# Kernel optimization log

Hardware: AMD Instinct MI355X
Metric: run time of the kernel (lower is better)

Reference implementation:

```python
import jax, jax.numpy as jnp
import numpy as np

B, T, C = 4, 2048, 2048
H, G = 16, 4            # num_heads, gqa_factor
HKV = H // G            # kv heads = 4
D = C // H              # head_dim = 128
KV = HKV * D            # kv_embed_dim = 512


def setup_inputs() -> dict:
    key = jax.random.key(0)
    ks = jax.random.split(key, 6)
    w_scale = (2.0 / (C + C)) ** 0.5  # xavier-uniform-ish std
    return {
        "query": jax.random.normal(ks[0], (B, T, C), jnp.float32),
        "key": jax.random.normal(ks[1], (B, T, C), jnp.float32),
        "value": jax.random.normal(ks[2], (B, T, C), jnp.float32),
        "in_proj_weight": jax.random.normal(ks[3], (C + 2 * KV, C), jnp.float32) * w_scale,
        "in_proj_bias": jnp.zeros((C + 2 * KV,), jnp.float32),
        "out_proj_weight": jax.random.normal(ks[4], (C, C), jnp.float32) * w_scale,
        "out_proj_bias": jnp.zeros((C,), jnp.float32),
    }


def reference(query, key, value, in_proj_weight, in_proj_bias, out_proj_weight, out_proj_bias):
    # split fused QKV projection (rows: [C | KV | KV])
    qw, kw, vw = in_proj_weight[:C], in_proj_weight[C:C + KV], in_proj_weight[C + KV:]
    qb, kb, vb = in_proj_bias[:C], in_proj_bias[C:C + KV], in_proj_bias[C + KV:]

    xq = query @ qw.T + qb          # (B,T,C)
    xk = key @ kw.T + kb            # (B,T,KV)
    xv = value @ vw.T + vb          # (B,T,KV)

    # (B,T,G,Hkv,D) -> (B,G,Hkv,T,D)
    xq = xq.reshape(B, T, G, HKV, D).transpose(0, 2, 3, 1, 4)
    # (B,T,Hkv,D) -> (B,Hkv,T,D); broadcast over G in attention
    xk = xk.reshape(B, T, HKV, D).transpose(0, 2, 1, 3)
    xv = xv.reshape(B, T, HKV, D).transpose(0, 2, 1, 3)

    scale = 1.0 / jnp.sqrt(jnp.asarray(D, xq.dtype))
    scores = jnp.einsum("bghtd,bhsd->bghts", xq, xk) * scale  # (B,G,Hkv,T,T)
    causal = jnp.tril(jnp.ones((T, T), bool))
    scores = jnp.where(causal, scores, jnp.finfo(scores.dtype).min)
    attn = jax.nn.softmax(scores, axis=-1)

    xo = jnp.einsum("bghts,bhsd->bghtd", attn, xv)            # (B,G,Hkv,T,D)
    xo = xo.transpose(0, 3, 1, 2, 4).reshape(B, T, C)          # (B,T,C)
    return xo @ out_proj_weight.T + out_proj_bias
```

## Files before the change

### kernel.cpp

```cpp
#include <hip/hip_runtime.h>
#include <hip/hip_bf16.h>
#include <stdint.h>

#define B_ 4
#define T_ 2048
#define C_ 2048
#define H_ 16
#define HKV_ 4
#define D_ 128
#define KV_ 512

typedef __attribute__((ext_vector_type(8))) short bf16x8;
typedef __attribute__((ext_vector_type(4))) float f32x4;

__device__ __forceinline__ unsigned short f2bf(float f) {
    union { float f; unsigned int u; } c;
    c.f = f;
    unsigned int u = c.u;
    u += 0x7FFFu + ((u >> 16) & 1u);
    return (unsigned short)(u >> 16);
}

__global__ __launch_bounds__(256)
void f32_to_bf16(const float* __restrict__ src, unsigned short* __restrict__ dst, int n4)
{
    int i = blockIdx.x * 256 + threadIdx.x;
    if (i < n4) {
        float4 v = ((const float4*)src)[i];
        ushort4 o;
        o.x = f2bf(v.x); o.y = f2bf(v.y); o.z = f2bf(v.z); o.w = f2bf(v.w);
        ((ushort4*)dst)[i] = o;
    }
}

template <typename OutT, bool TRANS>
__global__ __launch_bounds__(256)
void gemm_bt_bias(const __hip_bfloat16* __restrict__ A,
                  const __hip_bfloat16* __restrict__ W,
                  const float* __restrict__ bias,
                  OutT* __restrict__ Cmat,
                  int M, int N, int K)
{
    __shared__ __align__(16) __hip_bfloat16 lA[128 * 32];
    __shared__ __align__(16) __hip_bfloat16 lB[128 * 32];

    const int tid  = threadIdx.x;
    const int wave = tid >> 6;
    const int lane = tid & 63;
    const int m0 = blockIdx.x * 128;
    const int n0 = blockIdx.y * 128;
    const int wm = (wave >> 1) * 64;
    const int wn = (wave & 1) * 64;
    const int srow = lane >> 2;
    const int scol = (lane & 3) * 8;
    const int quad = lane >> 4;
    const int r16  = lane & 15;

    f32x4 acc[4][4];
#pragma unroll
    for (int i = 0; i < 4; ++i)
#pragma unroll
        for (int j = 0; j < 4; ++j)
            acc[i][j] = (f32x4){0.f, 0.f, 0.f, 0.f};

    const __hip_bfloat16* gA = A + (size_t)(m0 + wave * 16 + srow) * K + scol;
    const __hip_bfloat16* gB = W + (size_t)(n0 + wave * 16 + srow) * K + scol;

    for (int k0 = 0; k0 < K; k0 += 32) {
        __builtin_amdgcn_global_load_lds(
            (const __attribute__((address_space(1))) void*)(gA + k0),
            (__attribute__((address_space(3))) void*)(lA + wave * 16 * 32), 16, 0, 0);
        __builtin_amdgcn_global_load_lds(
            (const __attribute__((address_space(1))) void*)(gA + (size_t)64 * K + k0),
            (__attribute__((address_space(3))) void*)(lA + (64 + wave * 16) * 32), 16, 0, 0);
        __builtin_amdgcn_global_load_lds(
            (const __attribute__((address_space(1))) void*)(gB + k0),
            (__attribute__((address_space(3))) void*)(lB + wave * 16 * 32), 16, 0, 0);
        __builtin_amdgcn_global_load_lds(
            (const __attribute__((address_space(1))) void*)(gB + (size_t)64 * K + k0),
            (__attribute__((address_space(3))) void*)(lB + (64 + wave * 16) * 32), 16, 0, 0);
        __syncthreads();

        bf16x8 af[4], bfr[4];
#pragma unroll
        for (int i = 0; i < 4; ++i)
            af[i] = *(const bf16x8*)(lA + (wm + i * 16 + r16) * 32 + quad * 8);
#pragma unroll
        for (int j = 0; j < 4; ++j)
            bfr[j] = *(const bf16x8*)(lB + (wn + j * 16 + r16) * 32 + quad * 8);
#pragma unroll
        for (int i = 0; i < 4; ++i)
#pragma unroll
            for (int j = 0; j < 4; ++j)
                acc[i][j] = __builtin_amdgcn_mfma_f32_16x16x32_bf16(
                    af[i], bfr[j], acc[i][j], 0, 0, 0);
        __syncthreads();
    }

#pragma unroll
    for (int i = 0; i < 4; ++i) {
        const int row = m0 + wm + i * 16 + quad * 4;
#pragma unroll
        for (int j = 0; j < 4; ++j) {
            const int col = n0 + wn + j * 16 + r16;
            const float bb = bias[col];
            if constexpr (TRANS) {
                const int bb_idx = row >> 11;
                const int t = row & (T_ - 1);
                ushort4 o;
                o.x = f2bf(acc[i][j][0] + bb);
                o.y = f2bf(acc[i][j][1] + bb);
                o.z = f2bf(acc[i][j][2] + bb);
                o.w = f2bf(acc[i][j][3] + bb);
                *(ushort4*)((unsigned short*)Cmat +
                            ((size_t)(bb_idx * N + col)) * T_ + t) = o;
            } else {
#pragma unroll
                for (int r = 0; r < 4; ++r) {
                    const float v = acc[i][j][r] + bb;
                    if constexpr (sizeof(OutT) == 4) {
                        Cmat[(size_t)(row + r) * N + col] = v;
                    } else {
                        ((unsigned short*)Cmat)[(size_t)(row + r) * N + col] = f2bf(v);
                    }
                }
            }
        }
    }
}

__global__ __launch_bounds__(256)
void attn_flash(const __hip_bfloat16* __restrict__ xq,
                const __hip_bfloat16* __restrict__ xk,
                const __hip_bfloat16* __restrict__ xvT,
                __hip_bfloat16* __restrict__ xo)
{
    __shared__ __align__(16) __hip_bfloat16 lK[2][64 * 128];
    __shared__ __align__(16) __hip_bfloat16 lV[2][128 * 64];
    __shared__ __align__(16) __hip_bfloat16 lP[4 * 32 * 64];

    const int tid  = threadIdx.x;
    const int wave = tid >> 6;
    const int lane = tid & 63;
    const int quad = lane >> 4;
    const int r16  = lane & 15;
    const int sw8  = (r16 & 7) * 8;
    const int q0 = blockIdx.x * 128;
    const int h  = blockIdx.y;
    const int b  = blockIdx.z;
    const int hkv = h & (HKV_ - 1);
    const int r0 = q0 + wave * 32;
    const float scale = 0.08838834764831845f;
    const float SHIFT = 12.0f;

    bf16x8 qf[2][4];
#pragma unroll
    for (int i = 0; i < 2; ++i)
#pragma unroll
        for (int kc = 0; kc < 4; ++kc)
            qf[i][kc] = *(const bf16x8*)(
                xq + ((size_t)(b * T_ + r0 + i * 16 + r16)) * C_ +
                h * D_ + kc * 32 + quad * 8);

    f32x4 oacc[2][8];
#pragma unroll
    for (int i = 0; i < 2; ++i)
#pragma unroll
        for (int db = 0; db < 8; ++db)
            oacc[i][db] = (f32x4){0.f, 0.f, 0.f, 0.f};
    float lrow[2][4];
#pragma unroll
    for (int i = 0; i < 2; ++i)
#pragma unroll
        for (int r = 0; r < 4; ++r) lrow[i][r] = 0.f;

    const __hip_bfloat16* kb = xk + ((size_t)b * T_) * KV_ + hkv * D_;
    const __hip_bfloat16* vb = xvT + ((size_t)(b * KV_ + hkv * D_)) * T_;
    __hip_bfloat16* lPw = lP + wave * 32 * 64;

    const int vr   = lane >> 3;
    const int vsw  = ((lane & 7) ^ vr) * 8;

    const int ntiles = q0 / 64 + 2;

    auto STAGE = [&](int buf, int tile) {
        const int s0 = tile * 64;
        __hip_bfloat16* lKb = &lK[buf][0];
        __hip_bfloat16* lVb = &lV[buf][0];
#pragma unroll
        for (int q = 0; q < 4; ++q) {
            const int kr7 = (q * 4 + quad) & 7;
            __builtin_amdgcn_global_load_lds(
                (const __attribute__((address_space(1))) void*)(
                    kb + (size_t)(s0 + wave * 16 + q * 4 + quad) * KV_ +
                    ((r16 ^ kr7) * 8)),
                (__attribute__((address_space(3))) void*)(lKb + (wave * 16 + q * 4) * 128),
                16, 0, 0);
            __builtin_amdgcn_global_load_lds(
                (const __attribute__((address_space(1))) void*)(
                    vb + (size_t)(wave * 32 + q * 8 + vr) * T_ + s0 + vsw),
                (__attribute__((address_space(3))) void*)(lVb + (wave * 32 + q * 8) * 64),
                16, 0, 0);
        }
    };

    STAGE(0, 0);
    __syncthreads();

    for (int tile = 0; tile < ntiles; ++tile) {
        const int cur = tile & 1;
        const int s0 = tile * 64;

        if (tile + 1 < ntiles) STAGE(cur ^ 1, tile + 1);

        const __hip_bfloat16* lKc = &lK[cur][0];
        const __hip_bfloat16* lVc = &lV[cur][0];

        if (s0 <= r0 + 31) {
            const bool diag = (s0 + 63 > r0);

            f32x4 sacc[2][4];
#pragma unroll
            for (int i = 0; i < 2; ++i)
#pragma unroll
                for (int j = 0; j < 4; ++j)
                    sacc[i][j] = (f32x4){0.f, 0.f, 0.f, 0.f};
#pragma unroll
            for (int kc = 0; kc < 4; ++kc) {
                bf16x8 kf[4];
#pragma unroll
                for (int j = 0; j < 4; ++j)
                    kf[j] = *(const bf16x8*)(lKc + (j * 16 + r16) * 128 +
                                             ((kc * 32 + quad * 8) ^ sw8));
#pragma unroll
                for (int i = 0; i < 2; ++i)
#pragma unroll
                    for (int j = 0; j < 4; ++j)
                        sacc[i][j] = __builtin_amdgcn_mfma_f32_16x16x32_bf16(
                            qf[i][kc], kf[j], sacc[i][j], 0, 0, 0);
            }

#pragma unroll
            for (int i = 0; i < 2; ++i) {
#pragma unroll
                for (int j = 0; j < 4; ++j)
#pragma unroll
                    for (int r = 0; r < 4; ++r) {
                        float p = __expf(fmaf(sacc[i][j][r], scale, -SHIFT));
                        if (diag) {
                            const int rr = r0 + i * 16 + quad * 4 + r;
                            const int cc = s0 + j * 16 + r16;
                            if (cc > rr) p = 0.f;
                        }
                        lrow[i][r] += p;
                        const int prow = i * 16 + quad * 4 + r;
                        ((unsigned short*)lPw)[prow * 64 +
                            ((j * 16 + r16) ^ (((quad * 4 + r) & 7) * 8))] = f2bf(p);
                    }
            }

#pragma unroll
            for (int sc = 0; sc < 2; ++sc) {
                bf16x8 pf[2];
#pragma unroll
                for (int i = 0; i < 2; ++i)
                    pf[i] = *(const bf16x8*)(lPw + (i * 16 + r16) * 64 +
                                             ((sc * 32 + quad * 8) ^ sw8));
#pragma unroll
                for (int db = 0; db < 8; ++db) {
                    const bf16x8 vf = *(const bf16x8*)(lVc + (db * 16 + r16) * 64 +
                                                       ((sc * 32 + quad * 8) ^ sw8));
#pragma unroll
                    for (int i = 0; i < 2; ++i)
                        oacc[i][db] = __builtin_amdgcn_mfma_f32_16x16x32_bf16(
                            pf[i], vf, oacc[i][db], 0, 0, 0);
                }
            }
        }
        __syncthreads();
    }

#pragma unroll
    for (int i = 0; i < 2; ++i) {
#pragma unroll
        for (int off = 1; off <= 8; off <<= 1)
#pragma unroll
            for (int r = 0; r < 4; ++r)
                lrow[i][r] += __shfl_xor(lrow[i][r], off);
        float inv[4];
#pragma unroll
        for (int r = 0; r < 4; ++r) inv[r] = 1.0f / lrow[i][r];
#pragma unroll
        for (int db = 0; db < 8; ++db)
#pragma unroll
            for (int r = 0; r < 4; ++r)
                ((unsigned short*)xo)[((size_t)(b * T_ + r0 + i * 16 + quad * 4 + r)) * C_ +
                                      h * D_ + db * 16 + r16] =
                    f2bf(oacc[i][db][r] * inv[r]);
    }
}

extern "C" void kernel_launch(void* const* d_in, const int* in_sizes, int n_in,
                              void* d_out, int out_size, void* d_ws, size_t ws_size,
                              hipStream_t stream)
{
    const float* query = (const float*)d_in[0];
    const float* key   = (const float*)d_in[1];
    const float* value = (const float*)d_in[2];
    const float* ipw   = (const float*)d_in[3];
    const float* ipb   = (const float*)d_in[4];
    const float* opw   = (const float*)d_in[5];
    const float* opb   = (const float*)d_in[6];
    float* out = (float*)d_out;

    const size_t nQ  = (size_t)B_ * T_ * C_;
    const size_t nW  = (size_t)(C_ + 2 * KV_) * C_;
    const size_t nKV = (size_t)B_ * T_ * KV_;

    __hip_bfloat16* qb  = (__hip_bfloat16*)d_ws;
    __hip_bfloat16* wb  = qb + nQ;
    __hip_bfloat16* xq  = wb + nW;
    __hip_bfloat16* xk  = xq + nQ;
    __hip_bfloat16* xvT = xk + nKV;
    __hip_bfloat16* xo  = qb;

    const int M = B_ * T_;
    dim3 blk(256);

    f32_to_bf16<<<(int)(nW / 4 / 256), blk, 0, stream>>>(ipw, (unsigned short*)wb, (int)(nW / 4));
    f32_to_bf16<<<(int)(nQ / 4 / 256), blk, 0, stream>>>(query, (unsigned short*)qb, (int)(nQ / 4));
    gemm_bt_bias<__hip_bfloat16, false><<<dim3(M / 128, C_ / 128), blk, 0, stream>>>(
        qb, wb, ipb, xq, M, C_, C_);

    f32_to_bf16<<<(int)(nQ / 4 / 256), blk, 0, stream>>>(key, (unsigned short*)qb, (int)(nQ / 4));
    gemm_bt_bias<__hip_bfloat16, false><<<dim3(M / 128, KV_ / 128), blk, 0, stream>>>(
        qb, wb + (size_t)C_ * C_, ipb + C_, xk, M, KV_, C_);

    f32_to_bf16<<<(int)(nQ / 4 / 256), blk, 0, stream>>>(value, (unsigned short*)qb, (int)(nQ / 4));
    gemm_bt_bias<__hip_bfloat16, true><<<dim3(M / 128, KV_ / 128), blk, 0, stream>>>(
        qb, wb + (size_t)(C_ + KV_) * C_, ipb + C_ + KV_, xvT, M, KV_, C_);

    attn_flash<<<dim3(T_ / 128, H_, B_), blk, 0, stream>>>(xq, xk, xvT, xo);

    const size_t nOW = (size_t)C_ * C_;
    f32_to_bf16<<<(int)(nOW / 4 / 256), blk, 0, stream>>>(opw, (unsigned short*)wb, (int)(nOW / 4));
    gemm_bt_bias<float, false><<<dim3(M / 128, C_ / 128), blk, 0, stream>>>(
        xo, wb, opb, out, M, C_, C_);
}
```

Measured before the change: 747.7 us.

## Load V fragments directly into registers, reverse causal block order, use exp2

Removes the LDS staging buffer for V. Each wave now loads its V fragments straight from global memory into registers at the start of every tile, before the QK MFMAs, which cuts LDS traffic and footprint. Blocks are scheduled heaviest-first by reversing the query-tile order, the softmax exponent is folded into exp2 with pre-scaled constants, and launch bounds request two blocks per CU. The trade-off is that each wave redundantly fetches V from global/L2, adding latency and more register pressure.

```diff
diff --git a/kernel.cpp b/kernel.cpp
--- a/kernel.cpp
+++ b/kernel.cpp
@@ -129,15 +129,14 @@
     }
 }
 
-__global__ __launch_bounds__(256)
+__global__ __launch_bounds__(256, 2)
 void attn_flash(const __hip_bfloat16* __restrict__ xq,
                 const __hip_bfloat16* __restrict__ xk,
                 const __hip_bfloat16* __restrict__ xvT,
                 __hip_bfloat16* __restrict__ xo)
 {
     __shared__ __align__(16) __hip_bfloat16 lK[2][64 * 128];
-    __shared__ __align__(16) __hip_bfloat16 lV[2][128 * 64];
-    __shared__ __align__(16) __hip_bfloat16 lP[4 * 32 * 64];
+    __shared__ __align__(16) __hip_bfloat16 lP[4][32 * 64];
 
     const int tid  = threadIdx.x;
     const int wave = tid >> 6;
@@ -145,13 +144,13 @@
     const int quad = lane >> 4;
     const int r16  = lane & 15;
     const int sw8  = (r16 & 7) * 8;
-    const int q0 = blockIdx.x * 128;
+    const int q0 = (T_ / 128 - 1 - blockIdx.x) * 128;
     const int h  = blockIdx.y;
     const int b  = blockIdx.z;
     const int hkv = h & (HKV_ - 1);
     const int r0 = q0 + wave * 32;
-    const float scale = 0.08838834764831845f;
-    const float SHIFT = 12.0f;
+    const float SC2 = 0.12751879215f;
+    const float SH2 = 17.3123404907f;
 
     bf16x8 qf[2][4];
 #pragma unroll
@@ -176,17 +175,13 @@
 
     const __hip_bfloat16* kb = xk + ((size_t)b * T_) * KV_ + hkv * D_;
     const __hip_bfloat16* vb = xvT + ((size_t)(b * KV_ + hkv * D_)) * T_;
-    __hip_bfloat16* lPw = lP + wave * 32 * 64;
-
-    const int vr   = lane >> 3;
-    const int vsw  = ((lane & 7) ^ vr) * 8;
+    __hip_bfloat16* lPw = &lP[wave][0];
 
     const int ntiles = q0 / 64 + 2;
 
-    auto STAGE = [&](int buf, int tile) {
+    auto STAGE_K = [&](int buf, int tile) {
         const int s0 = tile * 64;
         __hip_bfloat16* lKb = &lK[buf][0];
-        __hip_bfloat16* lVb = &lV[buf][0];
 #pragma unroll
         for (int q = 0; q < 4; ++q) {
             const int kr7 = (q * 4 + quad) & 7;
@@ -196,27 +191,32 @@
                     ((r16 ^ kr7) * 8)),
                 (__attribute__((address_space(3))) void*)(lKb + (wave * 16 + q * 4) * 128),
                 16, 0, 0);
-            __builtin_amdgcn_global_load_lds(
-                (const __attribute__((address_space(1))) void*)(
-                    vb + (size_t)(wave * 32 + q * 8 + vr) * T_ + s0 + vsw),
-                (__attribute__((address_space(3))) void*)(lVb + (wave * 32 + q * 8) * 64),
-                16, 0, 0);
         }
     };
 
-    STAGE(0, 0);
+    STAGE_K(0, 0);
     __syncthreads();
 
     for (int tile = 0; tile < ntiles; ++tile) {
         const int cur = tile & 1;
         const int s0 = tile * 64;
 
-        if (tile + 1 < ntiles) STAGE(cur ^ 1, tile + 1);
+        if (tile + 1 < ntiles) STAGE_K(cur ^ 1, tile + 1);
 
         const __hip_bfloat16* lKc = &lK[cur][0];
-        const __hip_bfloat16* lVc = &lV[cur][0];
-
-        if (s0 <= r0 + 31) {
+        const bool active = (s0 <= r0 + 31);
+
+        bf16x8 vf[2][8];
+        if (active) {
+#pragma unroll
+            for (int sc = 0; sc < 2; ++sc)
+#pragma unroll
+                for (int db = 0; db < 8; ++db)
+                    vf[sc][db] = *(const bf16x8*)(
+                        vb + (size_t)(db * 16 + r16) * T_ + s0 + sc * 32 + quad * 8);
+        }
+
+        if (active) {
             const bool diag = (s0 + 63 > r0);
 
             f32x4 sacc[2][4];
@@ -246,7 +246,7 @@
                 for (int j = 0; j < 4; ++j)
 #pragma unroll
                     for (int r = 0; r < 4; ++r) {
-                        float p = __expf(fmaf(sacc[i][j][r], scale, -SHIFT));
+                        float p = exp2f(fmaf(sacc[i][j][r], SC2, -SH2));
                         if (diag) {
                             const int rr = r0 + i * 16 + quad * 4 + r;
                             const int cc = s0 + j * 16 + r16;
@@ -267,14 +267,11 @@
                     pf[i] = *(const bf16x8*)(lPw + (i * 16 + r16) * 64 +
                                              ((sc * 32 + quad * 8) ^ sw8));
 #pragma unroll
-                for (int db = 0; db < 8; ++db) {
-                    const bf16x8 vf = *(const bf16x8*)(lVc + (db * 16 + r16) * 64 +
-                                                       ((sc * 32 + quad * 8) ^ sw8));
+                for (int db = 0; db < 8; ++db)
 #pragma unroll
                     for (int i = 0; i < 2; ++i)
                         oacc[i][db] = __builtin_amdgcn_mfma_f32_16x16x32_bf16(
-                            pf[i], vf, oacc[i][db], 0, 0, 0);
-                }
+                            pf[i], vf[sc][db], oacc[i][db], 0, 0, 0);
             }
         }
         __syncthreads();
```

Measured after the change: 829.8 us. 11.0% more time.
